# Performance work log

Hardware: AMD Instinct MI355X
Metric: run time of the kernel (lower is better)

## Reference

```python
import jax, jax.numpy as jnp
import numpy as np

B, S, E = 8, 4096, 8          # batch, seq_len, embed_dim (= n_wires)
NUM_HEADS = 2
SCALE = 1.0 / np.sqrt(E // NUM_HEADS).astype(np.float32)  # 1/sqrt(d_k)


def setup_inputs() -> dict:
    key = jax.random.key(0)
    ks = jax.random.split(key, 10)
    s = 1.0 / np.sqrt(E)
    return {
        "x": jax.random.normal(ks[0], (B, S, E), dtype=jnp.float32),
        "Wq": jax.random.uniform(ks[1], (E, E), jnp.float32, -s, s),
        "bq": jax.random.uniform(ks[2], (E,), jnp.float32, -s, s),
        "Wk": jax.random.uniform(ks[3], (E, E), jnp.float32, -s, s),
        "bk": jax.random.uniform(ks[4], (E,), jnp.float32, -s, s),
        "Wv": jax.random.uniform(ks[5], (E, E), jnp.float32, -s, s),
        "bv": jax.random.uniform(ks[6], (E,), jnp.float32, -s, s),
        "theta": jax.random.normal(ks[7], (E,), dtype=jnp.float32),  # shared RX params (qkqv[0])
        "Wc": jax.random.uniform(ks[8], (E, E), jnp.float32, -s, s),
        "bc": jax.random.uniform(ks[9], (E,), jnp.float32, -s, s),
    }


def _qproj(h, theta):
    # RX(h_i) then RX(theta_i) on |0>, measure PauliZ: <Z_i> = cos(h_i + theta_i)
    return jnp.cos(h + theta)


def reference(x, Wq, bq, Wk, bk, Wv, bv, theta, Wc, bc):
    q = _qproj(x @ Wq.T + bq, theta)   # [B,S,E]
    k = _qproj(x @ Wk.T + bk, theta)
    v = _qproj(x @ Wv.T + bv, theta)
    scores = jnp.einsum('bse,bte->bst', q, k) * SCALE  # [B,S,S]
    attn = jax.nn.softmax(scores, axis=-1)             # dropout is identity in eval
    out = jnp.einsum('bst,bte->bse', attn, v)          # [B,S,E]
    return out @ Wc.T + bc
```

## Files before the change

### kernel.cpp

```cpp
#include <hip/hip_runtime.h>
#include <math.h>

#define E_DIM 8
#define S_DIM 4096
#define B_DIM 8
#define NROWS (B_DIM * S_DIM)
#define TCH 512
#define TSPLIT 4
#define VSTRIDE 520

#define QSCALE 0.72134752044448170f

typedef __attribute__((ext_vector_type(4))) float f4;
typedef __attribute__((ext_vector_type(2))) __fp16 h2;
typedef __attribute__((ext_vector_type(4))) __fp16 h4;
typedef __attribute__((ext_vector_type(8))) __fp16 h8;

union QU { uint2 u; h4 h; };
union H8U { h8 v; h2 p[4]; };

__device__ inline float fast_exp2(float x) {
#if __has_builtin(__builtin_amdgcn_exp2f)
    return __builtin_amdgcn_exp2f(x);
#else
    return exp2f(x);
#endif
}

__global__ __launch_bounds__(256) void qkv_kernel(
    const float* __restrict__ x,
    const float* __restrict__ Wq, const float* __restrict__ bq,
    const float* __restrict__ Wk, const float* __restrict__ bk,
    const float* __restrict__ Wv, const float* __restrict__ bv,
    const float* __restrict__ theta,
    uint4* __restrict__ Qh, uint4* __restrict__ Kg, __fp16* __restrict__ VTg)
{
    int tid = threadIdx.x;
    int half = tid >> 7;
    int row = blockIdx.x * 128 + (tid & 127);
    const float4* x4 = (const float4*)(x + (size_t)row * E_DIM);
    float4 xa = x4[0], xb = x4[1];
    float xr[8] = {xa.x, xa.y, xa.z, xa.w, xb.x, xb.y, xb.z, xb.w};

    int ib = half * 4;
    float q[4], k[4], v[4];
#pragma unroll
    for (int ii = 0; ii < 4; ++ii) {
        int i = ib + ii;
        float hq = bq[i], hk = bk[i], hv = bv[i];
#pragma unroll
        for (int j = 0; j < 8; ++j) {
            hq += xr[j] * Wq[i * 8 + j];
            hk += xr[j] * Wk[i * 8 + j];
            hv += xr[j] * Wv[i * 8 + j];
        }
        float th = theta[i];
        q[ii] = __cosf(hq + th) * QSCALE;
        k[ii] = __cosf(hk + th);
        v[ii] = __cosf(hv + th);
    }

    union { uint2 u; __fp16 s[4]; } qp, kp;
#pragma unroll
    for (int ii = 0; ii < 4; ++ii) { qp.s[ii] = (__fp16)q[ii]; kp.s[ii] = (__fp16)k[ii]; }
    ((uint2*)Qh)[(size_t)row * 2 + half] = qp.u;
    ((uint2*)Kg)[(size_t)row * 2 + half] = kp.u;

    int batch = row >> 12;
    int t = row & 4095;
#pragma unroll
    for (int e = 0; e < 4; ++e)
        VTg[((size_t)(batch * 8 + ib + e) << 12) + t] = (__fp16)v[e];
}

__global__ __launch_bounds__(256) void attn_mfma(
    const uint4* __restrict__ Qh, const uint4* __restrict__ Kg,
    const __fp16* __restrict__ VTg,
    float* __restrict__ ACC, float* __restrict__ DEN)
{
    __shared__ __align__(16) __fp16 Kpad[TCH * 16];
    __shared__ __align__(16) __fp16 Vt[16 * VSTRIDE];

    int tid = threadIdx.x;
    int l = tid & 63;
    int wv = tid >> 6;
    int rb = blockIdx.x;
    int sp = blockIdx.y;
    int batch = rb >> 5;
    int rbase = rb * 128 + wv * 32;

    for (int r = tid; r < TCH; r += 256)
        *((uint4*)(Kpad + r * 16 + 8)) = make_uint4(0, 0, 0, 0);
    {
        uint* z = (uint*)(Vt + 9 * VSTRIDE);
        for (int i = tid; i < 7 * VSTRIDE / 2; i += 256) z[i] = 0;
        uint* o1 = (uint*)(Vt + 8 * VSTRIDE);
        for (int i = tid; i < VSTRIDE / 2; i += 256) o1[i] = 0x3C003C00u;
    }

    QU q0u, q1u; q0u.u = make_uint2(0, 0); q1u.u = make_uint2(0, 0);
    if ((l >> 4) < 2) {
        const uint2* Q2 = (const uint2*)Qh;
        q0u.u = Q2[(size_t)(rbase + (l & 15)) * 2 + (l >> 4)];
        q1u.u = Q2[(size_t)(rbase + 16 + (l & 15)) * 2 + (l >> 4)];
    }
    h4 qf0 = q0u.h, qf1 = q1u.h;

    int koff = ((l & 12) << 1) + (l & 3);
    const __fp16* kbase = Kpad + (koff << 4) + ((l >> 4) << 2);
    const __fp16* vbase = Vt + (l & 15) * VSTRIDE + ((l >> 4) << 3);

    f4 C0 = {0.f, 0.f, 0.f, 0.f};
    f4 C1 = {0.f, 0.f, 0.f, 0.f};

    for (int ch = 0; ch < 1024 / TCH; ++ch) {
        int tb = sp * 1024 + ch * TCH;
        __syncthreads();
        {
            const uint4* src = Kg + ((size_t)batch << 12) + tb;
            for (int i = tid; i < TCH; i += 256)
                *((uint4*)(Kpad + i * 16)) = src[i];
        }
        {
            for (int i = tid; i < 8 * (TCH / 8); i += 256) {
                int e = i >> 6, c = i & 63;
                const uint4* src = (const uint4*)(VTg + (((size_t)(batch * 8 + e)) << 12) + tb);
                *((uint4*)(Vt + e * VSTRIDE + c * 8)) = src[c];
            }
        }
        __syncthreads();

#pragma unroll 4
        for (int ds = 0; ds < TCH / 32; ++ds) {
            h4 kf0 = *((const h4*)(kbase + ds * 512));
            h4 kf1 = *((const h4*)(kbase + ds * 512 + 64));
            h8 vr  = *((const h8*)(vbase + ds * 32));

            f4 z = {0.f, 0.f, 0.f, 0.f};
            f4 s00 = __builtin_amdgcn_mfma_f32_16x16x16f16(kf0, qf0, z, 0, 0, 0);
            f4 s01 = __builtin_amdgcn_mfma_f32_16x16x16f16(kf1, qf0, z, 0, 0, 0);
            f4 s10 = __builtin_amdgcn_mfma_f32_16x16x16f16(kf0, qf1, z, 0, 0, 0);
            f4 s11 = __builtin_amdgcn_mfma_f32_16x16x16f16(kf1, qf1, z, 0, 0, 0);

            f4 e00, e01, e10, e11;
#pragma unroll
            for (int i = 0; i < 4; ++i) {
                e00[i] = fast_exp2(s00[i]);
                e01[i] = fast_exp2(s01[i]);
                e10[i] = fast_exp2(s10[i]);
                e11[i] = fast_exp2(s11[i]);
            }
            H8U pa0, pa1;
            pa0.p[0] = __builtin_amdgcn_cvt_pkrtz(e00[0], e00[1]);
            pa0.p[1] = __builtin_amdgcn_cvt_pkrtz(e00[2], e00[3]);
            pa0.p[2] = __builtin_amdgcn_cvt_pkrtz(e01[0], e01[1]);
            pa0.p[3] = __builtin_amdgcn_cvt_pkrtz(e01[2], e01[3]);
            pa1.p[0] = __builtin_amdgcn_cvt_pkrtz(e10[0], e10[1]);
            pa1.p[1] = __builtin_amdgcn_cvt_pkrtz(e10[2], e10[3]);
            pa1.p[2] = __builtin_amdgcn_cvt_pkrtz(e11[0], e11[1]);
            pa1.p[3] = __builtin_amdgcn_cvt_pkrtz(e11[2], e11[3]);

            C0 = __builtin_amdgcn_mfma_f32_16x16x32_f16(pa0.v, vr, C0, 0, 0, 0);
            C1 = __builtin_amdgcn_mfma_f32_16x16x32_f16(pa1.v, vr, C1, 0, 0, 0);
        }
    }

    int e = l & 15;
    int g = l >> 4;
#pragma unroll
    for (int i = 0; i < 4; ++i) {
        int r0 = rbase + 4 * g + i;
        if (e < 8) {
            ACC[(((size_t)sp * NROWS + r0) << 3) + e] = C0[i];
            ACC[(((size_t)sp * NROWS + r0 + 16) << 3) + e] = C1[i];
        } else if (e == 8) {
            DEN[(size_t)sp * NROWS + r0] = C0[i];
            DEN[(size_t)sp * NROWS + r0 + 16] = C1[i];
        }
    }
}

__global__ __launch_bounds__(256) void finalize_kernel(
    const float* __restrict__ ACC, const float* __restrict__ DEN,
    const float* __restrict__ Wc, const float* __restrict__ bc,
    float* __restrict__ out)
{
    int row = blockIdx.x * blockDim.x + threadIdx.x;
    float a[8] = {0,0,0,0,0,0,0,0};
    float den = 0.f;
#pragma unroll
    for (int sp = 0; sp < TSPLIT; ++sp) {
        const float4* A4 = (const float4*)(ACC + (((size_t)sp * NROWS + row) << 3));
        float4 p0 = A4[0], p1 = A4[1];
        a[0] += p0.x; a[1] += p0.y; a[2] += p0.z; a[3] += p0.w;
        a[4] += p1.x; a[5] += p1.y; a[6] += p1.z; a[7] += p1.w;
        den += DEN[(size_t)sp * NROWS + row];
    }
    float inv = 1.0f / den;
#pragma unroll
    for (int j = 0; j < 8; ++j) a[j] *= inv;
    float r[8];
#pragma unroll
    for (int i = 0; i < 8; ++i) {
        float h = bc[i];
#pragma unroll
        for (int j = 0; j < 8; ++j) h += a[j] * Wc[i * 8 + j];
        r[i] = h;
    }
    float4* O4 = (float4*)(out + (size_t)row * 8);
    O4[0] = make_float4(r[0], r[1], r[2], r[3]);
    O4[1] = make_float4(r[4], r[5], r[6], r[7]);
}

extern "C" void kernel_launch(void* const* d_in, const int* in_sizes, int n_in,
                              void* d_out, int out_size, void* d_ws, size_t ws_size,
                              hipStream_t stream) {
    const float* x     = (const float*)d_in[0];
    const float* Wq    = (const float*)d_in[1];
    const float* bq    = (const float*)d_in[2];
    const float* Wk    = (const float*)d_in[3];
    const float* bk    = (const float*)d_in[4];
    const float* Wv    = (const float*)d_in[5];
    const float* bv    = (const float*)d_in[6];
    const float* theta = (const float*)d_in[7];
    const float* Wc    = (const float*)d_in[8];
    const float* bc    = (const float*)d_in[9];
    float* out = (float*)d_out;

    float* ws  = (float*)d_ws;
    uint4*  Qh  = (uint4*)ws;
    uint4*  Kg  = (uint4*)(ws + (size_t)NROWS * 4);
    __fp16* VTg = (__fp16*)(ws + (size_t)NROWS * 8);
    float*  ACC = ws + (size_t)NROWS * 12;
    float*  DEN = ACC + (size_t)TSPLIT * NROWS * 8;

    qkv_kernel<<<NROWS * 2 / 256, 256, 0, stream>>>(x, Wq, bq, Wk, bk, Wv, bv, theta, Qh, Kg, VTg);

    dim3 grid2(NROWS / 128, TSPLIT);
    attn_mfma<<<grid2, 256, 0, stream>>>(Qh, Kg, VTg, ACC, DEN);

    finalize_kernel<<<NROWS / 256, 256, 0, stream>>>(ACC, DEN, Wc, bc, out);
}
```

Baseline: 98.28 us.

## Fuse split-K finalize into attention kernel via last-block atomic counter

```diff
diff --git a/kernel.cpp b/kernel.cpp
--- a/kernel.cpp
+++ b/kernel.cpp
@@ -33,9 +33,11 @@
     const float* __restrict__ Wk, const float* __restrict__ bk,
     const float* __restrict__ Wv, const float* __restrict__ bv,
     const float* __restrict__ theta,
-    uint4* __restrict__ Qh, uint4* __restrict__ Kg, __fp16* __restrict__ VTg)
+    uint4* __restrict__ Qh, uint4* __restrict__ Kg, __fp16* __restrict__ VTg,
+    int* __restrict__ cnt)
 {
     int tid = threadIdx.x;
+    if (tid == 0) cnt[blockIdx.x] = 0;
     int half = tid >> 7;
     int row = blockIdx.x * 128 + (tid & 127);
     const float4* x4 = (const float4*)(x + (size_t)row * E_DIM);
@@ -76,10 +78,14 @@
 __global__ __launch_bounds__(256) void attn_mfma(
     const uint4* __restrict__ Qh, const uint4* __restrict__ Kg,
     const __fp16* __restrict__ VTg,
-    float* __restrict__ ACC, float* __restrict__ DEN)
+    float* __restrict__ ACC, float* __restrict__ DEN,
+    int* __restrict__ cnt,
+    const float* __restrict__ Wc, const float* __restrict__ bc,
+    float* __restrict__ out)
 {
     __shared__ __align__(16) __fp16 Kpad[TCH * 16];
     __shared__ __align__(16) __fp16 Vt[16 * VSTRIDE];
+    __shared__ int lastFlag;
 
     int tid = threadIdx.x;
     int l = tid & 63;
@@ -178,38 +184,43 @@
             DEN[(size_t)sp * NROWS + r0 + 16] = C1[i];
         }
     }
-}
-
-__global__ __launch_bounds__(256) void finalize_kernel(
-    const float* __restrict__ ACC, const float* __restrict__ DEN,
-    const float* __restrict__ Wc, const float* __restrict__ bc,
-    float* __restrict__ out)
-{
-    int row = blockIdx.x * blockDim.x + threadIdx.x;
-    float a[8] = {0,0,0,0,0,0,0,0};
-    float den = 0.f;
-#pragma unroll
-    for (int sp = 0; sp < TSPLIT; ++sp) {
-        const float4* A4 = (const float4*)(ACC + (((size_t)sp * NROWS + row) << 3));
-        float4 p0 = A4[0], p1 = A4[1];
-        a[0] += p0.x; a[1] += p0.y; a[2] += p0.z; a[3] += p0.w;
-        a[4] += p1.x; a[5] += p1.y; a[6] += p1.z; a[7] += p1.w;
-        den += DEN[(size_t)sp * NROWS + row];
-    }
-    float inv = 1.0f / den;
-#pragma unroll
-    for (int j = 0; j < 8; ++j) a[j] *= inv;
-    float r[8];
-#pragma unroll
-    for (int i = 0; i < 8; ++i) {
-        float h = bc[i];
-#pragma unroll
-        for (int j = 0; j < 8; ++j) h += a[j] * Wc[i * 8 + j];
-        r[i] = h;
-    }
-    float4* O4 = (float4*)(out + (size_t)row * 8);
-    O4[0] = make_float4(r[0], r[1], r[2], r[3]);
-    O4[1] = make_float4(r[4], r[5], r[6], r[7]);
+
+    __syncthreads();
+    if (tid == 0) {
+        __threadfence();
+        lastFlag = (atomicAdd(&cnt[rb], 1) == TSPLIT - 1);
+    }
+    __syncthreads();
+    if (lastFlag) {
+        __threadfence();
+        if (tid < 128) {
+            int row = rb * 128 + tid;
+            float a[8] = {0,0,0,0,0,0,0,0};
+            float den = 0.f;
+#pragma unroll
+            for (int s2 = 0; s2 < TSPLIT; ++s2) {
+                const float4* A4 = (const float4*)(ACC + (((size_t)s2 * NROWS + row) << 3));
+                float4 p0 = A4[0], p1 = A4[1];
+                a[0] += p0.x; a[1] += p0.y; a[2] += p0.z; a[3] += p0.w;
+                a[4] += p1.x; a[5] += p1.y; a[6] += p1.z; a[7] += p1.w;
+                den += DEN[(size_t)s2 * NROWS + row];
+            }
+            float inv = 1.0f / den;
+#pragma unroll
+            for (int j = 0; j < 8; ++j) a[j] *= inv;
+            float r[8];
+#pragma unroll
+            for (int i = 0; i < 8; ++i) {
+                float h = bc[i];
+#pragma unroll
+                for (int j = 0; j < 8; ++j) h += a[j] * Wc[i * 8 + j];
+                r[i] = h;
+            }
+            float4* O4 = (float4*)(out + (size_t)row * 8);
+            O4[0] = make_float4(r[0], r[1], r[2], r[3]);
+            O4[1] = make_float4(r[4], r[5], r[6], r[7]);
+        }
+    }
 }
 
 extern "C" void kernel_launch(void* const* d_in, const int* in_sizes, int n_in,
@@ -233,11 +244,11 @@
     __fp16* VTg = (__fp16*)(ws + (size_t)NROWS * 8);
     float*  ACC = ws + (size_t)NROWS * 12;
     float*  DEN = ACC + (size_t)TSPLIT * NROWS * 8;
-
-    qkv_kernel<<<NROWS * 2 / 256, 256, 0, stream>>>(x, Wq, bq, Wk, bk, Wv, bv, theta, Qh, Kg, VTg);
+    int*    cnt = (int*)(DEN + (size_t)TSPLIT * NROWS);
+
+    qkv_kernel<<<NROWS * 2 / 256, 256, 0, stream>>>(x, Wq, bq, Wk, bk, Wv, bv, theta,
+                                                    Qh, Kg, VTg, cnt);
 
     dim3 grid2(NROWS / 128, TSPLIT);
-    attn_mfma<<<grid2, 256, 0, stream>>>(Qh, Kg, VTg, ACC, DEN);
-
-    finalize_kernel<<<NROWS / 256, 256, 0, stream>>>(ACC, DEN, Wc, bc, out);
-}
+    attn_mfma<<<grid2, 256, 0, stream>>>(Qh, Kg, VTg, ACC, DEN, cnt, Wc, bc, out);
+}
```

Measured after the change: 140.1 us. +42.6%, slower.
